# Kernel optimization log

Hardware: AMD Instinct MI355X
Metric: run time of the kernel (lower is better)

The kernel has to match this reference:

```python
import jax, jax.numpy as jnp
import numpy as np

NUM_EMBEDDINGS = 8192
EMBEDDING_DIM = 256
COMMITMENT_COST = 0.25


def setup_inputs() -> dict:
    key = jax.random.key(0)
    k1, k2 = jax.random.split(key)
    inputs = jax.random.normal(k1, (16, EMBEDDING_DIM, 32, 32), dtype=jnp.float32)
    # nn.Embedding weight init: uniform(-1/num_embeddings, 1/num_embeddings)
    emb = jax.random.uniform(
        k2, (NUM_EMBEDDINGS, EMBEDDING_DIM), dtype=jnp.float32,
        minval=-1.0 / NUM_EMBEDDINGS, maxval=1.0 / NUM_EMBEDDINGS)
    return {"inputs": inputs, "emb": emb}


def reference(inputs, emb):
    # b c h w -> b h w c
    x = jnp.transpose(inputs, (0, 2, 3, 1))
    b, h, w, c = x.shape
    flat = x.reshape(-1, c)  # [N, c], N = b*h*w

    distances = (jnp.sum(flat * flat, axis=1, keepdims=True)
                 + jnp.sum(emb * emb, axis=1)
                 - 2.0 * jnp.matmul(flat, emb.T))
    encoding_indices = jnp.argmin(distances, axis=1)  # [N]
    encodings = jax.nn.one_hot(encoding_indices, NUM_EMBEDDINGS, dtype=flat.dtype)  # [N, K]

    # gather-via-matmul, as in the original
    quantized = jnp.matmul(encodings, emb).reshape(b, h, w, c)

    sg = jax.lax.stop_gradient
    e_latent_loss = jnp.mean((sg(quantized) - x) ** 2)
    q_latent_loss = jnp.mean((quantized - sg(x)) ** 2)
    loss = q_latent_loss + COMMITMENT_COST * e_latent_loss

    # straight-through estimator
    quantized_st = x + sg(quantized - x)

    avg_probs = jnp.mean(encodings, axis=0)  # [K]
    perplexity = jnp.exp(-jnp.sum(avg_probs * jnp.log(avg_probs + 1e-10)))

    # back to b c h w (intended layout of the returned quantized tensor)
    quantized_out = jnp.transpose(quantized_st, (0, 3, 1, 2))
    return loss, quantized_out, perplexity, encodings
```

## Files before the change

### kernel.cpp

```cpp
#include <hip/hip_runtime.h>
#include <math.h>

#define N_ROWS   16384
#define K_EMB    8192
#define C_DIM    256
#define QUANT_N  4194304
#define QUANT_OFF 1
#define PERP_OFF  4194305
#define ENC_OFF   4194306

#define CAND_CAP 128

#define WS_BK    0
#define WS_AN    8192
#define WS_AMIN  24576
#define WS_CCNT  57344
#define WS_CAND  73728
#define WS_IDX   4268032
#define WS_CNT   4284416
#define WS_ACC   4292608
#define WS_XH    4292616
#define WS_EH    6389768

typedef __attribute__((ext_vector_type(8))) short short8_t;
typedef __attribute__((ext_vector_type(4))) float f32x4;
typedef __attribute__((ext_vector_type(8))) unsigned short u16x8;
typedef unsigned long long ull;

__device__ __forceinline__ unsigned short f2bf(float f) {
    unsigned int u = __float_as_uint(f);
    u += 0x7FFFu + ((u >> 16) & 1u);
    return (unsigned short)(u >> 16);
}

__global__ void vq_init_kernel(ull* __restrict__ amin, unsigned int* __restrict__ ccnt,
                               int* __restrict__ counts, double* __restrict__ acc) {
    int t = blockIdx.x * 256 + threadIdx.x;
    amin[t] = 0xFFFFFFFFFFFFFFFFull;
    ccnt[t] = 0u;
    if (t < K_EMB) counts[t] = 0;
    if (t == 0) acc[0] = 0.0;
}

__global__ void vq_bk_kernel(const float* __restrict__ emb, float* __restrict__ bk) {
    int row  = blockIdx.x * 4 + (threadIdx.x >> 6);
    int lane = threadIdx.x & 63;
    float4 v = reinterpret_cast<const float4*>(emb)[(size_t)row * 64 + lane];
    float s = v.x * v.x + v.y * v.y + v.z * v.z + v.w * v.w;
#pragma unroll
    for (int o = 32; o > 0; o >>= 1) s += __shfl_down(s, o, 64);
    if (lane == 0) bk[row] = s;
}

__global__ void vq_an_kernel(const float* __restrict__ xin, float* __restrict__ an) {
    int n = blockIdx.x * 256 + threadIdx.x;
    int b = n >> 10, hw = n & 1023;
    const float* xr = xin + (size_t)b * (C_DIM * 1024) + hw;
    float s = 0.f;
    for (int c = 0; c < C_DIM; ++c) { float v = xr[(size_t)c * 1024]; s = fmaf(v, v, s); }
    an[n] = s;
}

__global__ void vq_packx_kernel(const float* __restrict__ xin, unsigned short* __restrict__ xh) {
    __shared__ float tile[64][65];
    const int t = threadIdx.x;
    const int nb = blockIdx.x >> 2;
    const int cb = blockIdx.x & 3;
    const int n0 = nb * 64;
    const int b  = n0 >> 10, hw0 = n0 & 1023;
    {
        int cl = t >> 6, nl = t & 63;
#pragma unroll
        for (int i = 0; i < 16; ++i) {
            int c = cb * 64 + cl * 16 + i;
            tile[cl * 16 + i][nl] = xin[(size_t)b * (C_DIM * 1024) + (size_t)c * 1024 + hw0 + nl];
        }
    }
    __syncthreads();
    {
        int nl = t >> 2, cq = t & 3;
#pragma unroll
        for (int j = 0; j < 2; ++j) {
            u16x8 v;
#pragma unroll
            for (int jj = 0; jj < 8; ++jj) v[jj] = f2bf(tile[cq * 16 + j * 8 + jj][nl]);
            *reinterpret_cast<u16x8*>(&xh[(size_t)(n0 + nl) * 256 + cb * 64 + cq * 16 + j * 8]) = v;
        }
    }
}

__global__ void vq_packe_kernel(const float* __restrict__ emb, unsigned short* __restrict__ eh) {
    int flat = blockIdx.x * 256 + threadIdx.x;
    int k = flat >> 4, c16 = flat & 15;
    const float4* src = reinterpret_cast<const float4*>(emb) + (size_t)k * 64 + c16 * 4;
#pragma unroll
    for (int j = 0; j < 2; ++j) {
        float4 v0 = src[j * 2], v1 = src[j * 2 + 1];
        u16x8 v;
        v[0]=f2bf(v0.x); v[1]=f2bf(v0.y); v[2]=f2bf(v0.z); v[3]=f2bf(v0.w);
        v[4]=f2bf(v1.x); v[5]=f2bf(v1.y); v[6]=f2bf(v1.z); v[7]=f2bf(v1.w);
        *reinterpret_cast<u16x8*>(&eh[(size_t)k * 256 + c16 * 16 + j * 8]) = v;
    }
}

__launch_bounds__(256, 2)
__global__ void vq_mfma_kernel(const unsigned short* __restrict__ xh,
                               const unsigned short* __restrict__ eh,
                               const float* __restrict__ an,
                               const float* __restrict__ bk,
                               ull* __restrict__ amin,
                               unsigned int* __restrict__ ccnt,
                               ull* __restrict__ cand,
                               float* __restrict__ enc) {
    __shared__ unsigned short e_lds[256][72];
    __shared__ unsigned short x_lds[128][72];
    __shared__ ull key_lds[128][4];
    const int t  = threadIdx.x;
    const int rb = blockIdx.x >> 5;
    const int kb = blockIdx.x & 31;
    const int w  = t >> 6;
    const int l  = t & 63;
    const int lr = l & 15;
    const int lg = l >> 4;

    f32x4 acc[4][8];
#pragma unroll
    for (int kt = 0; kt < 4; ++kt)
#pragma unroll
        for (int rt = 0; rt < 8; ++rt) acc[kt][rt] = (f32x4){0.f, 0.f, 0.f, 0.f};

    const unsigned short* xbase = xh + (size_t)(rb * 128) * 256;
    const unsigned short* ebase = eh + (size_t)(kb * 256) * 256;
    float2* enc_z = reinterpret_cast<float2*>(enc + (size_t)blockIdx.x * 32768);

    for (int cc = 0; cc < 4; ++cc) {
        __syncthreads();
#pragma unroll
        for (int i = 0; i < 8; ++i) {
            int flat = t + 256 * i;
            int kr = flat >> 3, u8 = flat & 7;
            *reinterpret_cast<u16x8*>(&e_lds[kr][u8 * 8]) =
                *reinterpret_cast<const u16x8*>(&ebase[(size_t)kr * 256 + cc * 64 + u8 * 8]);
        }
#pragma unroll
        for (int i = 0; i < 4; ++i) {
            int flat = t + 256 * i;
            int xr = flat >> 3, u8 = flat & 7;
            *reinterpret_cast<u16x8*>(&x_lds[xr][u8 * 8]) =
                *reinterpret_cast<const u16x8*>(&xbase[(size_t)xr * 256 + cc * 64 + u8 * 8]);
        }
#pragma unroll
        for (int z = 0; z < 16; ++z)
            enc_z[(cc * 16 + z) * 256 + t] = (float2){0.f, 0.f};
        __syncthreads();
#pragma unroll
        for (int step = 0; step < 2; ++step) {
            const int cl = step * 32 + lg * 8;
            short8_t af[4], bf[8];
#pragma unroll
            for (int kt = 0; kt < 4; ++kt)
                af[kt] = *reinterpret_cast<const short8_t*>(&e_lds[w * 64 + kt * 16 + lr][cl]);
#pragma unroll
            for (int rt = 0; rt < 8; ++rt)
                bf[rt] = *reinterpret_cast<const short8_t*>(&x_lds[rt * 16 + lr][cl]);
#pragma unroll
            for (int kt = 0; kt < 4; ++kt)
#pragma unroll
                for (int rt = 0; rt < 8; ++rt)
                    acc[kt][rt] = __builtin_amdgcn_mfma_f32_16x16x32_bf16(af[kt], bf[rt], acc[kt][rt], 0, 0, 0);
        }
    }

    float bvals[16];
#pragma unroll
    for (int kt = 0; kt < 4; ++kt)
#pragma unroll
        for (int reg = 0; reg < 4; ++reg)
            bvals[kt * 4 + reg] = bk[kb * 256 + w * 64 + kt * 16 + lg * 4 + reg];

    float ar8[8];
#pragma unroll
    for (int rt = 0; rt < 8; ++rt) {
        const int row = rb * 128 + rt * 16 + lr;
        const float a_r = an[row];
        ar8[rt] = a_r;
        float mn = 3.402823466e38f; int mk = 0;
#pragma unroll
        for (int kt = 0; kt < 4; ++kt)
#pragma unroll
            for (int reg = 0; reg < 4; ++reg) {
                float d = fmaf(-2.f, acc[kt][rt][reg], a_r + bvals[kt * 4 + reg]);
                acc[kt][rt][reg] = d;
                int k = kb * 256 + w * 64 + kt * 16 + lg * 4 + reg;
                if (d < mn) { mn = d; mk = k; }
            }
        ull key = ((ull)__float_as_uint(mn) << 32) | (unsigned)mk;
        ull o1 = __shfl_xor(key, 16, 64); if (o1 < key) key = o1;
        ull o2 = __shfl_xor(key, 32, 64); if (o2 < key) key = o2;
        if (lg == 0) key_lds[rt * 16 + lr][w] = key;
    }
    __syncthreads();
#pragma unroll
    for (int rt = 0; rt < 8; ++rt) {
        const int row = rb * 128 + rt * 16 + lr;
        ull bmin = key_lds[rt * 16 + lr][0];
#pragma unroll
        for (int j = 1; j < 4; ++j) { ull v = key_lds[rt * 16 + lr][j]; if (v < bmin) bmin = v; }
        if (w == 0 && lg == 0) atomicMin(&amin[row], bmin);
        ull obs = amin[row];
        if (obs < bmin) bmin = obs;
        float md  = __uint_as_float((unsigned)(bmin >> 32));
        float thr = md + fmaf(4.0e-5f, sqrtf(ar8[rt]), 1.6e-4f);
#pragma unroll
        for (int kt = 0; kt < 4; ++kt)
#pragma unroll
            for (int reg = 0; reg < 4; ++reg) {
                float d = acc[kt][rt][reg];
                if (d <= thr) {
                    int k = kb * 256 + w * 64 + kt * 16 + lg * 4 + reg;
                    unsigned pos = atomicAdd(&ccnt[row], 1u);
                    if (pos < CAND_CAP)
                        cand[(size_t)row * CAND_CAP + pos] =
                            ((ull)__float_as_uint(d) << 32) | (unsigned)k;
                }
            }
    }
}

__global__ void vq_select_kernel(const float* __restrict__ xin,
                                 const float* __restrict__ emb,
                                 const float* __restrict__ an,
                                 const float* __restrict__ bk,
                                 const ull* __restrict__ amin,
                                 const unsigned int* __restrict__ ccnt,
                                 const ull* __restrict__ cand,
                                 int* __restrict__ idx_ws,
                                 int* __restrict__ counts,
                                 float* __restrict__ enc) {
    __shared__ float xrow4[256][4];
    const int t = threadIdx.x;
    const int w = t >> 6, l = t & 63;
    const int n0 = blockIdx.x * 4;
    const int b  = n0 >> 10, hw0 = n0 & 1023;
    {
        float4 v = *reinterpret_cast<const float4*>(
            xin + (size_t)b * (C_DIM * 1024) + (size_t)t * 1024 + hw0);
        xrow4[t][0] = v.x; xrow4[t][1] = v.y; xrow4[t][2] = v.z; xrow4[t][3] = v.w;
    }
    __syncthreads();

    const int r = n0 + w;
    const unsigned cnt = ccnt[r];
    const float a_r = an[r];
    const float glob = __uint_as_float((unsigned)(amin[r] >> 32));
    const float thr  = glob + fmaf(4.0e-5f, sqrtf(a_r), 1.6e-4f);

    ull mykey = 0xFFFFFFFFFFFFFFFFull;
    if (cnt <= CAND_CAP) {
        for (unsigned i = l; i < cnt; i += 64) {
            ull e64 = cand[(size_t)r * CAND_CAP + i];
            float dt = __uint_as_float((unsigned)(e64 >> 32));
            if (dt <= thr) {
                int k = (int)(unsigned)(e64 & 0xFFFFFFFFull);
                const float* e = emb + (size_t)k * C_DIM;
                float m = 0.f;
                for (int c = 0; c < C_DIM; ++c) m = fmaf(xrow4[c][w], e[c], m);
                float d = fmaf(-2.f, m, a_r + bk[k]);
                ull key = ((ull)__float_as_uint(d) << 32) | (unsigned)k;
                if (key < mykey) mykey = key;
            }
        }
    } else {
        for (int k = l; k < K_EMB; k += 64) {
            const float* e = emb + (size_t)k * C_DIM;
            float m = 0.f;
            for (int c = 0; c < C_DIM; ++c) m = fmaf(xrow4[c][w], e[c], m);
            float d = fmaf(-2.f, m, a_r + bk[k]);
            ull key = ((ull)__float_as_uint(d) << 32) | (unsigned)k;
            if (key < mykey) mykey = key;
        }
    }
#pragma unroll
    for (int o = 32; o > 0; o >>= 1) {
        ull ok = __shfl_xor(mykey, o, 64);
        if (ok < mykey) mykey = ok;
    }
    if (l == 0) {
        int bi = (int)(unsigned)(mykey & 0xFFFFFFFFull);
        idx_ws[r] = bi;
        atomicAdd(&counts[bi], 1);
        enc[(size_t)r * K_EMB + bi] = 1.0f;
    }
}

__global__ void vq_quant_loss_kernel(const float* __restrict__ xin,
                                     const float* __restrict__ emb,
                                     const int* __restrict__ idx_ws,
                                     float* __restrict__ out,
                                     double* __restrict__ acc) {
    __shared__ float q_lds[64][257];
    __shared__ int   k_lds[64];
    const int tid = threadIdx.x;
    const int n0  = blockIdx.x * 64;
    const int b_img = n0 >> 10;
    const int hw0   = n0 & 1023;

    if (tid < 64) k_lds[tid] = idx_ws[n0 + tid];
    __syncthreads();
#pragma unroll
    for (int p = 0; p < 16; ++p) {
        int idx = tid + p * 256;
        int row = idx >> 6;
        int c4  = idx & 63;
        float4 q = reinterpret_cast<const float4*>(emb)[(size_t)k_lds[row] * 64 + c4];
        q_lds[row][c4 * 4 + 0] = q.x;
        q_lds[row][c4 * 4 + 1] = q.y;
        q_lds[row][c4 * 4 + 2] = q.z;
        q_lds[row][c4 * 4 + 3] = q.w;
    }
    __syncthreads();

    double local = 0.0;
    const size_t base = (size_t)b_img * (C_DIM * 1024) + hw0;
    const int hw = tid & 63;
    const int cb = tid >> 6;
    for (int pass = 0; pass < 64; ++pass) {
        int c = pass * 4 + cb;
        size_t off = base + (size_t)c * 1024 + hw;
        float x = xin[off];
        float q = q_lds[hw][c];
        float dq = q - x;
        out[QUANT_OFF + off] = x + dq;
        local += (double)dq * (double)dq;
    }
#pragma unroll
    for (int o = 32; o > 0; o >>= 1) local += __shfl_down(local, o, 64);
    __shared__ double wsum[4];
    if ((threadIdx.x & 63) == 0) wsum[threadIdx.x >> 6] = local;
    __syncthreads();
    if (threadIdx.x == 0) atomicAdd(acc, wsum[0] + wsum[1] + wsum[2] + wsum[3]);
}

__global__ void vq_finalize_kernel(const int* __restrict__ counts,
                                   const double* __restrict__ acc,
                                   float* __restrict__ out) {
    double s = 0.0;
    for (int k = threadIdx.x; k < K_EMB; k += 256) {
        int c = counts[k];
        if (c > 0) {
            double p = (double)c * (1.0 / 16384.0);
            s += p * log(p + 1e-10);
        }
    }
#pragma unroll
    for (int o = 32; o > 0; o >>= 1) s += __shfl_down(s, o, 64);
    __shared__ double wsum[4];
    if ((threadIdx.x & 63) == 0) wsum[threadIdx.x >> 6] = s;
    __syncthreads();
    if (threadIdx.x == 0) {
        double tot = wsum[0] + wsum[1] + wsum[2] + wsum[3];
        out[PERP_OFF] = (float)exp(-tot);
        float l = (float)(acc[0] * (1.0 / (double)QUANT_N));
        out[0] = l + 0.25f * l;
    }
}

extern "C" void kernel_launch(void* const* d_in, const int* in_sizes, int n_in,
                              void* d_out, int out_size, void* d_ws, size_t ws_size,
                              hipStream_t stream) {
    const float* xin = (const float*)d_in[0];
    const float* emb = (const float*)d_in[1];
    float* out = (float*)d_out;
    float* ws  = (float*)d_ws;

    float*          bk     = ws + WS_BK;
    float*          an     = ws + WS_AN;
    ull*            amin   = (ull*)(ws + WS_AMIN);
    unsigned int*   ccnt   = (unsigned int*)(ws + WS_CCNT);
    ull*            cand   = (ull*)(ws + WS_CAND);
    int*            idx_ws = (int*)(ws + WS_IDX);
    int*            counts = (int*)(ws + WS_CNT);
    double*         acc    = (double*)(ws + WS_ACC);
    unsigned short* xh     = (unsigned short*)(ws + WS_XH);
    unsigned short* eh     = (unsigned short*)(ws + WS_EH);

    vq_init_kernel<<<64, 256, 0, stream>>>(amin, ccnt, counts, acc);
    vq_bk_kernel<<<K_EMB / 4, 256, 0, stream>>>(emb, bk);
    vq_an_kernel<<<N_ROWS / 256, 256, 0, stream>>>(xin, an);
    vq_packe_kernel<<<(K_EMB * 16) / 256, 256, 0, stream>>>(emb, eh);
    vq_packx_kernel<<<(N_ROWS / 64) * 4, 256, 0, stream>>>(xin, xh);
    vq_mfma_kernel<<<128 * 32, 256, 0, stream>>>(xh, eh, an, bk, amin, ccnt, cand, out + ENC_OFF);
    vq_select_kernel<<<N_ROWS / 4, 256, 0, stream>>>(xin, emb, an, bk, amin, ccnt, cand,
                                                     idx_ws, counts, out + ENC_OFF);
    vq_quant_loss_kernel<<<N_ROWS / 64, 256, 0, stream>>>(xin, emb, idx_ws, out, acc);
    vq_finalize_kernel<<<1, 256, 0, stream>>>(counts, acc, out);
}
```

Baseline: 937.0 us.

## Load embeddings directly into registers, stage full x tile once, memset encodings

The MFMA kernel now stages the whole 128x256 x tile in LDS once, with no per-chunk barriers. Each wave reads its embedding fragments straight from global memory into registers instead of going through LDS. Zeroing of the one-hot encodings moves out of the GEMM kernel into a hipMemsetAsync. The re-read of the global argmin after the atomic is also dropped, so the candidate threshold uses only the block-local minimum. This may admit more candidates per row and risks overflowing the candidate cap. Larger LDS use for x may also lower occupancy.

```diff
diff --git a/kernel.cpp b/kernel.cpp
--- a/kernel.cpp
+++ b/kernel.cpp
@@ -110,10 +110,8 @@
                                const float* __restrict__ bk,
                                ull* __restrict__ amin,
                                unsigned int* __restrict__ ccnt,
-                               ull* __restrict__ cand,
-                               float* __restrict__ enc) {
-    __shared__ unsigned short e_lds[256][72];
-    __shared__ unsigned short x_lds[128][72];
+                               ull* __restrict__ cand) {
+    __shared__ unsigned short x_lds[128][264];
     __shared__ ull key_lds[128][4];
     const int t  = threadIdx.x;
     const int rb = blockIdx.x >> 5;
@@ -123,43 +121,36 @@
     const int lr = l & 15;
     const int lg = l >> 4;
 
+    const unsigned short* xbase = xh + (size_t)(rb * 128) * 256;
+#pragma unroll
+    for (int i = 0; i < 16; ++i) {
+        int chunk = t + 256 * i;
+        int row = chunk >> 5, c8 = chunk & 31;
+        *reinterpret_cast<u16x8*>(&x_lds[row][c8 * 8]) =
+            *reinterpret_cast<const u16x8*>(&xbase[(size_t)row * 256 + c8 * 8]);
+    }
+    __syncthreads();
+
     f32x4 acc[4][8];
 #pragma unroll
     for (int kt = 0; kt < 4; ++kt)
 #pragma unroll
         for (int rt = 0; rt < 8; ++rt) acc[kt][rt] = (f32x4){0.f, 0.f, 0.f, 0.f};
 
-    const unsigned short* xbase = xh + (size_t)(rb * 128) * 256;
-    const unsigned short* ebase = eh + (size_t)(kb * 256) * 256;
-    float2* enc_z = reinterpret_cast<float2*>(enc + (size_t)blockIdx.x * 32768);
+    const unsigned short* eptr = eh + (size_t)(kb * 256 + w * 64 + lr) * 256 + lg * 8;
 
     for (int cc = 0; cc < 4; ++cc) {
-        __syncthreads();
-#pragma unroll
-        for (int i = 0; i < 8; ++i) {
-            int flat = t + 256 * i;
-            int kr = flat >> 3, u8 = flat & 7;
-            *reinterpret_cast<u16x8*>(&e_lds[kr][u8 * 8]) =
-                *reinterpret_cast<const u16x8*>(&ebase[(size_t)kr * 256 + cc * 64 + u8 * 8]);
-        }
-#pragma unroll
-        for (int i = 0; i < 4; ++i) {
-            int flat = t + 256 * i;
-            int xr = flat >> 3, u8 = flat & 7;
-            *reinterpret_cast<u16x8*>(&x_lds[xr][u8 * 8]) =
-                *reinterpret_cast<const u16x8*>(&xbase[(size_t)xr * 256 + cc * 64 + u8 * 8]);
-        }
-#pragma unroll
-        for (int z = 0; z < 16; ++z)
-            enc_z[(cc * 16 + z) * 256 + t] = (float2){0.f, 0.f};
-        __syncthreads();
+        u16x8 af[2][4];
+#pragma unroll
+        for (int step = 0; step < 2; ++step)
+#pragma unroll
+            for (int kt = 0; kt < 4; ++kt)
+                af[step][kt] = *reinterpret_cast<const u16x8*>(
+                    eptr + (size_t)kt * 16 * 256 + cc * 64 + step * 32);
 #pragma unroll
         for (int step = 0; step < 2; ++step) {
-            const int cl = step * 32 + lg * 8;
-            short8_t af[4], bf[8];
-#pragma unroll
-            for (int kt = 0; kt < 4; ++kt)
-                af[kt] = *reinterpret_cast<const short8_t*>(&e_lds[w * 64 + kt * 16 + lr][cl]);
+            const int cl = cc * 64 + step * 32 + lg * 8;
+            short8_t bf[8];
 #pragma unroll
             for (int rt = 0; rt < 8; ++rt)
                 bf[rt] = *reinterpret_cast<const short8_t*>(&x_lds[rt * 16 + lr][cl]);
@@ -167,7 +158,8 @@
             for (int kt = 0; kt < 4; ++kt)
 #pragma unroll
                 for (int rt = 0; rt < 8; ++rt)
-                    acc[kt][rt] = __builtin_amdgcn_mfma_f32_16x16x32_bf16(af[kt], bf[rt], acc[kt][rt], 0, 0, 0);
+                    acc[kt][rt] = __builtin_amdgcn_mfma_f32_16x16x32_bf16(
+                        (short8_t)af[step][kt], bf[rt], acc[kt][rt], 0, 0, 0);
         }
     }
 
@@ -207,8 +199,6 @@
 #pragma unroll
         for (int j = 1; j < 4; ++j) { ull v = key_lds[rt * 16 + lr][j]; if (v < bmin) bmin = v; }
         if (w == 0 && lg == 0) atomicMin(&amin[row], bmin);
-        ull obs = amin[row];
-        if (obs < bmin) bmin = obs;
         float md  = __uint_as_float((unsigned)(bmin >> 32));
         float thr = md + fmaf(4.0e-5f, sqrtf(ar8[rt]), 1.6e-4f);
 #pragma unroll
@@ -384,12 +374,13 @@
     unsigned short* xh     = (unsigned short*)(ws + WS_XH);
     unsigned short* eh     = (unsigned short*)(ws + WS_EH);
 
+    hipMemsetAsync(out + ENC_OFF, 0, (size_t)N_ROWS * K_EMB * sizeof(float), stream);
     vq_init_kernel<<<64, 256, 0, stream>>>(amin, ccnt, counts, acc);
     vq_bk_kernel<<<K_EMB / 4, 256, 0, stream>>>(emb, bk);
     vq_an_kernel<<<N_ROWS / 256, 256, 0, stream>>>(xin, an);
     vq_packe_kernel<<<(K_EMB * 16) / 256, 256, 0, stream>>>(emb, eh);
     vq_packx_kernel<<<(N_ROWS / 64) * 4, 256, 0, stream>>>(xin, xh);
-    vq_mfma_kernel<<<128 * 32, 256, 0, stream>>>(xh, eh, an, bk, amin, ccnt, cand, out + ENC_OFF);
+    vq_mfma_kernel<<<128 * 32, 256, 0, stream>>>(xh, eh, an, bk, amin, ccnt, cand);
     vq_select_kernel<<<N_ROWS / 4, 256, 0, stream>>>(xin, emb, an, bk, amin, ccnt, cand,
                                                      idx_ws, counts, out + ENC_OFF);
     vq_quant_loss_kernel<<<N_ROWS / 64, 256, 0, stream>>>(xin, emb, idx_ws, out, acc);
```

Result: slower. 1.657 ms (+76.9%).
